# Kernel optimization log

Measured on AMD Instinct MI355X. Metric: run time of the kernel, lower is better.

Reference implementation:

```python
import jax, jax.numpy as jnp
import numpy as np

N = 100000   # nodes
E = 1000000  # edges
IN, H, OUT = 256, 64, 16


def setup_inputs() -> dict:
    key = jax.random.key(0)
    k0, k1, k2, k3 = jax.random.split(key, 4)
    x = jax.random.normal(k0, (N, IN), jnp.float32)
    edge_index = jax.random.randint(k1, (2, E), 0, N)
    # GCNConv parameters (glorot-ish weights, zero bias as in PyG defaults)
    W1 = jax.random.normal(k2, (IN, H), jnp.float32) / np.sqrt(IN).astype(np.float32)
    b1 = jnp.zeros((H,), jnp.float32)
    W2 = jax.random.normal(k3, (H, OUT), jnp.float32) / np.sqrt(H).astype(np.float32)
    b2 = jnp.zeros((OUT,), jnp.float32)
    return {"x": x, "edge_index": edge_index, "W1": W1, "b1": b1, "W2": W2, "b2": b2}


def gcn_conv(x, W, b, src, dst, n):
    # PyG GCNConv: h = x @ W; out[v] = sum_{(u->v)} norm(u,v) * h[u] + b
    h = x @ W                                    # [n, out]
    deg = jnp.zeros((n,), h.dtype).at[dst].add(1.0)
    dinv = jnp.where(deg > 0, jax.lax.rsqrt(deg), 0.0)
    norm = dinv[src] * dinv[dst]                 # [E+n] symmetric normalization
    msg = h[src] * norm[:, None]                 # gather + scale
    agg = jax.ops.segment_sum(msg, dst, num_segments=n)  # scatter-add
    return agg + b


def reference(x, edge_index, W1, b1, W2, b2):
    n = x.shape[0]
    # add self-loops (PyG GCNConv default add_self_loops=True)
    loops = jnp.arange(n, dtype=edge_index.dtype)
    src = jnp.concatenate([edge_index[0], loops])
    dst = jnp.concatenate([edge_index[1], loops])
    h = gcn_conv(x, W1, b1, src, dst, n)
    h = jax.nn.relu(h)  # F.dropout is identity in eval mode (training=False)
    return gcn_conv(h, W2, b2, src, dst, n)
```

## Files before the change

### kernel.cpp

```cpp
#include <hip/hip_runtime.h>

namespace {
constexpr int NN  = 100000;
constexpr int NE  = 1000000;
constexpr int INF = 256;
constexpr int HF  = 64;
constexpr int OF  = 16;
constexpr int SCAN_CHUNK = 1024;
constexpr int NBLK = (NN + SCAN_CHUNK - 1) / SCAN_CHUNK;
constexpr int NSEG = 8;
constexpr int SEGW = (NN + NSEG - 1) / NSEG;
constexpr int CNTW = 100096;
constexpr int ZBLK = (CNTW / 4 + 255) / 256;
}

typedef __attribute__((ext_vector_type(8))) short     sh8;
typedef __attribute__((ext_vector_type(4))) float     f32x4;
typedef __attribute__((ext_vector_type(8))) unsigned short us8;

__device__ __forceinline__ unsigned short f2bf(float f) {
    unsigned int u = __builtin_bit_cast(unsigned int, f);
    u += 0x7FFFu + ((u >> 16) & 1u);
    return (unsigned short)(u >> 16);
}
__device__ __forceinline__ float bf2f(unsigned short s) {
    return __builtin_bit_cast(float, (unsigned int)s << 16);
}

__global__ void k_pre(int* __restrict__ cnt, const float* __restrict__ W1,
                      unsigned short* __restrict__ wt_g) {
    int b = blockIdx.x, t = threadIdx.x;
    if (b < ZBLK) {
        int i = (b * 256 + t) * 4;
        if (i < CNTW) *(int4*)(cnt + i) = (int4){0, 0, 0, 0};
    } else {
        int idx = (b - ZBLK) * 256 + t;
        int c = idx >> 8, k = idx & 255;
        wt_g[idx] = f2bf(W1[(size_t)k * HF + c]);
    }
}

__global__ void k_hist(const int* __restrict__ dst, int* __restrict__ cnt) {
    int b     = blockIdx.x;
    int seg   = b & (NSEG - 1);
    int chunk = b >> 3;
    int e = chunk * 256 + threadIdx.x;
    if (e < NE) {
        int d = dst[e];
        if ((unsigned)d / (unsigned)SEGW == (unsigned)seg)
            atomicAdd(&cnt[d], 1);
    }
}

__global__ __launch_bounds__(256) void k_reduce(const int* __restrict__ cnt,
                                                int* __restrict__ bsum,
                                                float* __restrict__ dinv) {
    int t = threadIdx.x;
    int i0 = blockIdx.x * SCAN_CHUNK + t * 4;
    int s = 0;
    float dv[4] = {0.f, 0.f, 0.f, 0.f};
    #pragma unroll
    for (int q = 0; q < 4; ++q) {
        if (i0 + q < NN) {
            int c = cnt[i0 + q];
            s += c;
            dv[q] = rsqrtf((float)(c + 1));
        }
    }
    if (i0 + 3 < NN) *(float4*)(dinv + i0) = (float4){dv[0], dv[1], dv[2], dv[3]};
    else { for (int q = 0; q < 4; ++q) if (i0 + q < NN) dinv[i0 + q] = dv[q]; }
    #pragma unroll
    for (int off = 32; off > 0; off >>= 1) s += __shfl_down(s, off);
    __shared__ int wsum[4];
    int lane = t & 63, wid = t >> 6;
    if (lane == 0) wsum[wid] = s;
    __syncthreads();
    if (t == 0) bsum[blockIdx.x] = wsum[0] + wsum[1] + wsum[2] + wsum[3];
}

__global__ void k_partials(int* __restrict__ bsum) {
    int l = threadIdx.x;
    int a0 = (l < NBLK) ? bsum[l] : 0;
    int b0 = (64 + l < NBLK) ? bsum[64 + l] : 0;
    int a = a0, b = b0;
    #pragma unroll
    for (int off = 1; off < 64; off <<= 1) {
        int na = __shfl_up(a, off); if (l >= off) a += na;
        int nb = __shfl_up(b, off); if (l >= off) b += nb;
    }
    int tot = __shfl(a, 63);
    if (l < NBLK) bsum[l] = a - a0;
    if (64 + l < NBLK) bsum[64 + l] = tot + b - b0;
}

__global__ __launch_bounds__(256) void k_scan(const int* __restrict__ cnt,
                                              const int* __restrict__ bsum,
                                              int* __restrict__ rowptr,
                                              int* __restrict__ cursor) {
    int t = threadIdx.x;
    int i0 = blockIdx.x * SCAN_CHUNK + t * 4;
    int v0 = 0, v1 = 0, v2 = 0, v3 = 0;
    if (i0 + 0 < NN) v0 = cnt[i0 + 0];
    if (i0 + 1 < NN) v1 = cnt[i0 + 1];
    if (i0 + 2 < NN) v2 = cnt[i0 + 2];
    if (i0 + 3 < NN) v3 = cnt[i0 + 3];
    int tsum = v0 + v1 + v2 + v3;
    int lane = t & 63, wid = t >> 6;
    int incl = tsum;
    #pragma unroll
    for (int off = 1; off < 64; off <<= 1) {
        int n = __shfl_up(incl, off);
        if (lane >= off) incl += n;
    }
    __shared__ int wsum[4];
    if (lane == 63) wsum[wid] = incl;
    __syncthreads();
    int woff = 0;
    for (int w = 0; w < wid; ++w) woff += wsum[w];
    int excl = woff + (incl - tsum) + bsum[blockIdx.x];
    int e0 = excl, e1 = e0 + v0, e2 = e1 + v1, e3 = e2 + v2;
    if (i0 + 0 < NN) { rowptr[i0 + 0] = e0; cursor[i0 + 0] = e0; }
    if (i0 + 1 < NN) { rowptr[i0 + 1] = e1; cursor[i0 + 1] = e1; }
    if (i0 + 2 < NN) { rowptr[i0 + 2] = e2; cursor[i0 + 2] = e2; }
    if (i0 + 3 < NN) { rowptr[i0 + 3] = e3; cursor[i0 + 3] = e3; }
    if (i0 + 3 == NN - 1) rowptr[NN] = e3 + v3;
}

__global__ __launch_bounds__(256) void k_scatter(const int* __restrict__ src,
                                                 const int* __restrict__ dst,
                                                 int* __restrict__ cursor,
                                                 int* __restrict__ eidx) {
    int b     = blockIdx.x;
    int seg   = b & (NSEG - 1);
    int chunk = b >> 3;
    int e = chunk * 256 + threadIdx.x;
    if (e < NE) {
        int d = dst[e];
        if ((unsigned)d / (unsigned)SEGW == (unsigned)seg) {
            int p = atomicAdd(&cursor[d], 1);
            eidx[p] = src[e];
        }
    }
}

__global__ __launch_bounds__(256, 4) void k_gemm1(const float* __restrict__ x,
                                                  const unsigned short* __restrict__ wt_g,
                                                  unsigned short* __restrict__ h1) {
    __shared__ unsigned short wt[64 * 264];
    int t = threadIdx.x;
    int w = t >> 6, l = t & 63;
    int row0 = blockIdx.x * 128;

    #pragma unroll
    for (int p = 0; p < 8; ++p) {
        int T   = p * 256 + t;
        int c   = T >> 5;
        int kb8 = T & 31;
        *(us8*)(wt + c * 264 + kb8 * 8) = *(const us8*)(wt_g + c * 256 + kb8 * 8);
    }
    __syncthreads();

    int m = l & 15;
    int g = l >> 4;
    int gr0 = row0 + w * 32 + m;      if (gr0 > NN - 1) gr0 = NN - 1;
    int gr1 = row0 + w * 32 + 16 + m; if (gr1 > NN - 1) gr1 = NN - 1;
    const float* p0 = x + (size_t)gr0 * INF + g * 8;
    const float* p1 = x + (size_t)gr1 * INF + g * 8;

    f32x4 acc[2][4];
    #pragma unroll
    for (int i = 0; i < 2; ++i)
        #pragma unroll
        for (int j = 0; j < 4; ++j) acc[i][j] = (f32x4){0.f, 0.f, 0.f, 0.f};

    #pragma unroll 2
    for (int kb = 0; kb < INF; kb += 32) {
        float4 u0 = *(const float4*)(p0 + kb);
        float4 u1 = *(const float4*)(p0 + kb + 4);
        float4 u2 = *(const float4*)(p1 + kb);
        float4 u3 = *(const float4*)(p1 + kb + 4);
        us8 a0u = { f2bf(u0.x), f2bf(u0.y), f2bf(u0.z), f2bf(u0.w),
                    f2bf(u1.x), f2bf(u1.y), f2bf(u1.z), f2bf(u1.w) };
        us8 a1u = { f2bf(u2.x), f2bf(u2.y), f2bf(u2.z), f2bf(u2.w),
                    f2bf(u3.x), f2bf(u3.y), f2bf(u3.z), f2bf(u3.w) };
        sh8 a0 = __builtin_bit_cast(sh8, a0u);
        sh8 a1 = __builtin_bit_cast(sh8, a1u);
        #pragma unroll
        for (int nt = 0; nt < 4; ++nt) {
            sh8 b = *(const sh8*)(wt + (nt * 16 + m) * 264 + kb + g * 8);
            acc[0][nt] = __builtin_amdgcn_mfma_f32_16x16x32_bf16(a0, b, acc[0][nt], 0, 0, 0);
            acc[1][nt] = __builtin_amdgcn_mfma_f32_16x16x32_bf16(a1, b, acc[1][nt], 0, 0, 0);
        }
    }

    #pragma unroll
    for (int mt = 0; mt < 2; ++mt) {
        #pragma unroll
        for (int r = 0; r < 4; ++r) {
            int gr = row0 + w * 32 + mt * 16 + (l >> 4) * 4 + r;
            if (gr < NN) {
                #pragma unroll
                for (int nt = 0; nt < 4; ++nt)
                    h1[(size_t)gr * HF + nt * 16 + (l & 15)] = f2bf(acc[mt][nt][r]);
            }
        }
    }
}

__global__ __launch_bounds__(256) void k_gather1(const int* __restrict__ rowptr,
                                                 const int* __restrict__ eidx,
                                                 const float* __restrict__ dinv,
                                                 const unsigned short* __restrict__ h1,
                                                 const float* __restrict__ b1,
                                                 const float* __restrict__ W2,
                                                 float* __restrict__ h2) {
    __shared__ float w2L[HF * OF];
    __shared__ float hrL[32][HF + 4];
    int t = threadIdx.x;
    *(float4*)(w2L + t * 4) = *(const float4*)(W2 + t * 4);

    int nodeL = t >> 3;
    int fg    = t & 7;
    int v     = blockIdx.x * 32 + nodeL;
    int beg = rowptr[v], end = rowptr[v + 1];

    float acc[8] = {};
    for (int i = beg; i < end; ++i) {
        int s = eidx[i];
        float wgt = dinv[s];
        us8 hv = *(const us8*)(h1 + (size_t)s * HF + fg * 8);
        #pragma unroll
        for (int q = 0; q < 8; ++q) acc[q] += wgt * bf2f(hv[q]);
    }

    {
        float dv = dinv[v], sl = dv * dv;
        us8 hv = *(const us8*)(h1 + (size_t)v * HF + fg * 8);
        #pragma unroll
        for (int q = 0; q < 8; ++q) {
            float val = dv * acc[q] + sl * bf2f(hv[q]) + b1[fg * 8 + q];
            hrL[nodeL][fg * 8 + q] = val > 0.f ? val : 0.f;
        }
    }
    __syncthreads();

    #pragma unroll
    for (int T = t; T < 512; T += 256) {
        int n = T >> 4, j = T & 15;
        const float* hr = hrL[n];
        float p = 0.f;
        #pragma unroll
        for (int k = 0; k < HF; ++k) p += hr[k] * w2L[k * OF + j];
        h2[(size_t)(blockIdx.x * 32 + n) * OF + j] = p;
    }
}

__global__ __launch_bounds__(256) void k_gather2(const int* __restrict__ rowptr,
                                                 const int* __restrict__ eidx,
                                                 const float* __restrict__ dinv,
                                                 const float* __restrict__ h2,
                                                 const float* __restrict__ b2,
                                                 float* __restrict__ out) {
    int gid   = blockIdx.x * 256 + threadIdx.x;
    int v     = gid >> 6;
    int lane  = threadIdx.x & 63;
    int eslot = lane >> 2;
    int fg    = lane & 3;
    int beg = rowptr[v], end = rowptr[v + 1];
    float4 acc = {0.f, 0.f, 0.f, 0.f};
    for (int i = beg + eslot; i < end; i += 16) {
        int s = eidx[i];
        float w = dinv[s];
        float4 hv = *(const float4*)(h2 + (size_t)s * OF + fg * 4);
        acc.x += w * hv.x; acc.y += w * hv.y; acc.z += w * hv.z; acc.w += w * hv.w;
    }
    #pragma unroll
    for (int m = 4; m <= 32; m <<= 1) {
        acc.x += __shfl_xor(acc.x, m);
        acc.y += __shfl_xor(acc.y, m);
        acc.z += __shfl_xor(acc.z, m);
        acc.w += __shfl_xor(acc.w, m);
    }
    if (eslot == 0) {
        float dv = dinv[v];
        float sl = dv * dv;
        float4 hv = *(const float4*)(h2 + (size_t)v * OF + fg * 4);
        float4 bv = *(const float4*)(b2 + fg * 4);
        float4 o;
        o.x = dv * acc.x + sl * hv.x + bv.x;
        o.y = dv * acc.y + sl * hv.y + bv.y;
        o.z = dv * acc.z + sl * hv.z + bv.z;
        o.w = dv * acc.w + sl * hv.w + bv.w;
        *(float4*)(out + (size_t)v * OF + fg * 4) = o;
    }
}

extern "C" void kernel_launch(void* const* d_in, const int* in_sizes, int n_in,
                              void* d_out, int out_size, void* d_ws, size_t ws_size,
                              hipStream_t stream) {
    const float* x   = (const float*)d_in[0];
    const int*   ei  = (const int*)d_in[1];
    const int*   src = ei;
    const int*   dst = ei + NE;
    const float* W1  = (const float*)d_in[2];
    const float* b1  = (const float*)d_in[3];
    const float* W2  = (const float*)d_in[4];
    const float* b2  = (const float*)d_in[5];
    float* out = (float*)d_out;

    float* dinv  = (float*)d_ws;
    unsigned short* h1b = (unsigned short*)(dinv + CNTW);
    float* h2    = (float*)(h1b + (size_t)NN * HF);
    int*   cnt   = (int*)(h2 + (size_t)NN * OF);
    int*   rowptr = cnt + CNTW;
    int*   cursor = rowptr + 100352;
    int*   eidx  = cursor + CNTW;
    int*   bsum  = eidx + NE;
    unsigned short* wt_g = (unsigned short*)(bsum + 128);

    k_pre<<<ZBLK + 64, 256, 0, stream>>>(cnt, W1, wt_g);
    k_hist<<<((NE + 255) / 256) * NSEG, 256, 0, stream>>>(dst, cnt);
    k_reduce<<<NBLK, 256, 0, stream>>>(cnt, bsum, dinv);
    k_partials<<<1, 64, 0, stream>>>(bsum);
    k_scan<<<NBLK, 256, 0, stream>>>(cnt, bsum, rowptr, cursor);
    k_scatter<<<((NE + 255) / 256) * NSEG, 256, 0, stream>>>(src, dst, cursor, eidx);

    k_gemm1<<<(NN + 127) / 128, 256, 0, stream>>>(x, wt_g, h1b);
    k_gather1<<<NN / 32, 256, 0, stream>>>(rowptr, eidx, dinv, h1b, b1, W2, h2);

    k_gather2<<<(NN * HF) / 256, 256, 0, stream>>>(rowptr, eidx, dinv, h2, b2, out);
}
```

Measured before the change: 188.5 us.

## Pre-partition edges into destination segments before histogram and scatter

Adds a partition kernel that buckets each (src,dst) pair into one of eight destination-range segments using block-local shared counters and one global atomic per segment. The histogram and scatter kernels then read only their own segment's compacted list instead of every block scanning the full edge array and discarding seven eighths of it. This removes redundant reads of dst/src (8x over-read) at the cost of an extra pass writing and reading an 8-byte-per-edge buffer. It also relies on a fixed per-segment capacity of 131072, which holds only if destinations are spread roughly evenly across segments.

Measured after the change: 200.9 us. 1.07x slower.

```diff
diff --git a/kernel.cpp b/kernel.cpp
--- a/kernel.cpp
+++ b/kernel.cpp
@@ -12,6 +12,8 @@
 constexpr int SEGW = (NN + NSEG - 1) / NSEG;
 constexpr int CNTW = 100096;
 constexpr int ZBLK = (CNTW / 4 + 255) / 256;
+constexpr int CAP  = 131072;
+constexpr int HSBLK = NSEG * (CAP / 256);
 }
 
 typedef __attribute__((ext_vector_type(8))) short     sh8;
@@ -28,27 +30,51 @@
 }
 
 __global__ void k_pre(int* __restrict__ cnt, const float* __restrict__ W1,
-                      unsigned short* __restrict__ wt_g) {
+                      unsigned short* __restrict__ wt_g, int* __restrict__ segcnt) {
     int b = blockIdx.x, t = threadIdx.x;
     if (b < ZBLK) {
         int i = (b * 256 + t) * 4;
         if (i < CNTW) *(int4*)(cnt + i) = (int4){0, 0, 0, 0};
     } else {
+        if (b == ZBLK && t < NSEG) segcnt[t] = 0;
         int idx = (b - ZBLK) * 256 + t;
         int c = idx >> 8, k = idx & 255;
         wt_g[idx] = f2bf(W1[(size_t)k * HF + c]);
     }
 }
 
-__global__ void k_hist(const int* __restrict__ dst, int* __restrict__ cnt) {
-    int b     = blockIdx.x;
-    int seg   = b & (NSEG - 1);
-    int chunk = b >> 3;
-    int e = chunk * 256 + threadIdx.x;
-    if (e < NE) {
-        int d = dst[e];
-        if ((unsigned)d / (unsigned)SEGW == (unsigned)seg)
-            atomicAdd(&cnt[d], 1);
+__global__ __launch_bounds__(1024) void k_part(const int* __restrict__ src,
+                                               const int* __restrict__ dst,
+                                               int2* __restrict__ segbuf,
+                                               int* __restrict__ segcnt) {
+    __shared__ int cnt8[NSEG];
+    __shared__ int base8[NSEG];
+    int t = threadIdx.x;
+    if (t < NSEG) cnt8[t] = 0;
+    __syncthreads();
+    int e = blockIdx.x * 1024 + t;
+    int s = 0, d = 0, seg = 0, rank = 0;
+    bool ok = e < NE;
+    if (ok) {
+        s = src[e]; d = dst[e];
+        seg = (unsigned)d / (unsigned)SEGW;
+        rank = atomicAdd(&cnt8[seg], 1);
+    }
+    __syncthreads();
+    if (t < NSEG) base8[t] = atomicAdd(&segcnt[t], cnt8[t]);
+    __syncthreads();
+    if (ok) segbuf[seg * CAP + base8[seg] + rank] = make_int2(s, d);
+}
+
+__global__ __launch_bounds__(256) void k_hist(const int2* __restrict__ segbuf,
+                                              const int* __restrict__ segcnt,
+                                              int* __restrict__ cnt) {
+    int b   = blockIdx.x;
+    int seg = b & (NSEG - 1);
+    int i   = (b >> 3) * 256 + threadIdx.x;
+    if (i < segcnt[seg]) {
+        int d = segbuf[seg * CAP + i].y;
+        atomicAdd(&cnt[d], 1);
     }
 }
 
@@ -126,20 +152,17 @@
     if (i0 + 3 == NN - 1) rowptr[NN] = e3 + v3;
 }
 
-__global__ __launch_bounds__(256) void k_scatter(const int* __restrict__ src,
-                                                 const int* __restrict__ dst,
+__global__ __launch_bounds__(256) void k_scatter(const int2* __restrict__ segbuf,
+                                                 const int* __restrict__ segcnt,
                                                  int* __restrict__ cursor,
                                                  int* __restrict__ eidx) {
-    int b     = blockIdx.x;
-    int seg   = b & (NSEG - 1);
-    int chunk = b >> 3;
-    int e = chunk * 256 + threadIdx.x;
-    if (e < NE) {
-        int d = dst[e];
-        if ((unsigned)d / (unsigned)SEGW == (unsigned)seg) {
-            int p = atomicAdd(&cursor[d], 1);
-            eidx[p] = src[e];
-        }
+    int b   = blockIdx.x;
+    int seg = b & (NSEG - 1);
+    int i   = (b >> 3) * 256 + threadIdx.x;
+    if (i < segcnt[seg]) {
+        int2 ed = segbuf[seg * CAP + i];
+        int p = atomicAdd(&cursor[ed.y], 1);
+        eidx[p] = ed.x;
     }
 }
 
@@ -317,13 +340,16 @@
     int*   eidx  = cursor + CNTW;
     int*   bsum  = eidx + NE;
     unsigned short* wt_g = (unsigned short*)(bsum + 128);
-
-    k_pre<<<ZBLK + 64, 256, 0, stream>>>(cnt, W1, wt_g);
-    k_hist<<<((NE + 255) / 256) * NSEG, 256, 0, stream>>>(dst, cnt);
+    int*   segcnt = (int*)(wt_g + 64 * 256);
+    int2*  segbuf = (int2*)(segcnt + 8);
+
+    k_pre<<<ZBLK + 64, 256, 0, stream>>>(cnt, W1, wt_g, segcnt);
+    k_part<<<(NE + 1023) / 1024, 1024, 0, stream>>>(src, dst, segbuf, segcnt);
+    k_hist<<<HSBLK, 256, 0, stream>>>(segbuf, segcnt, cnt);
     k_reduce<<<NBLK, 256, 0, stream>>>(cnt, bsum, dinv);
     k_partials<<<1, 64, 0, stream>>>(bsum);
     k_scan<<<NBLK, 256, 0, stream>>>(cnt, bsum, rowptr, cursor);
-    k_scatter<<<((NE + 255) / 256) * NSEG, 256, 0, stream>>>(src, dst, cursor, eidx);
+    k_scatter<<<HSBLK, 256, 0, stream>>>(segbuf, segcnt, cursor, eidx);
 
     k_gemm1<<<(NN + 127) / 128, 256, 0, stream>>>(x, wt_g, h1b);
     k_gather1<<<NN / 32, 256, 0, stream>>>(rowptr, eidx, dinv, h1b, b1, W2, h2);
```
